# Optimization experiments

Measured on AMD Instinct MI355X. Metric: run time of the kernel, lower is better.

The kernel has to match this reference:

```python
import jax, jax.numpy as jnp
import numpy as np

D_MODEL = 1024
N_HEADS = 16
D_K = D_MODEL // N_HEADS
THETA = 10000.0
BATCH, SEQ = 2, 2048


def setup_inputs() -> dict:
    key = jax.random.key(0)
    k1, k2, k3 = jax.random.split(key, 3)
    std_qkv = float(np.sqrt(2.0 / (3 * D_MODEL + D_MODEL)))
    std_o = float(np.sqrt(2.0 / (D_MODEL + D_MODEL)))
    return {
        "x": jax.random.normal(k1, (BATCH, SEQ, D_MODEL), dtype=jnp.float32),
        "w_qkv": jax.random.normal(k2, (3 * D_MODEL, D_MODEL), dtype=jnp.float32) * std_qkv,
        "w_o": jax.random.normal(k3, (D_MODEL, D_MODEL), dtype=jnp.float32) * std_o,
        "token_positions": jnp.arange(SEQ, dtype=jnp.int32),
    }


def _rope(x, token_positions):
    # x: [..., s, d_k]; interleaved rotary embedding
    d_k = x.shape[-1]
    freqs = jnp.arange(0, d_k, 2, dtype=jnp.float32) / d_k          # [d_k/2]
    inv_freqs = 1.0 / (THETA ** freqs)
    angles = token_positions.astype(jnp.float32)[:, None] * inv_freqs  # [s, d_k/2]
    cos, sin = jnp.cos(angles), jnp.sin(angles)
    x_even, x_odd = x[..., 0::2], x[..., 1::2]
    rot_even = x_even * cos - x_odd * sin
    rot_odd = x_even * sin + x_odd * cos
    # interleave back: out[..., 2i] = rot_even[i], out[..., 2i+1] = rot_odd[i]
    return jnp.stack([rot_even, rot_odd], axis=-1).reshape(x.shape)


def reference(x, w_qkv, w_o, token_positions):
    b, s, _ = x.shape
    qkv = jnp.einsum('oi,bsi->bso', w_qkv, x)                        # [b, s, 3*d_model]
    q, k, v = jnp.split(qkv, 3, axis=-1)
    def to_heads(t):
        return t.reshape(b, s, N_HEADS, D_K).transpose(0, 2, 1, 3)  # [b, h, s, d]
    q, k, v = to_heads(q), to_heads(k), to_heads(v)
    q = _rope(q, token_positions)
    k = _rope(k, token_positions)
    scores = jnp.einsum('bhqd,bhkd->bhqk', q, k) / jnp.sqrt(jnp.float32(D_K))
    causal = jnp.tril(jnp.ones((s, s), dtype=bool))
    scores = jnp.where(causal, scores, -jnp.inf)
    attn = jax.nn.softmax(scores, axis=-1)
    y = jnp.einsum('bhqk,bhkd->bhqd', attn, v)
    y = y.transpose(0, 2, 1, 3).reshape(b, s, D_MODEL)
    return jnp.einsum('oi,bsi->bso', w_o, y)
```

## Files before the change

### kernel.cpp

```cpp
#include <hip/hip_runtime.h>
#include <math.h>

#define DEV __device__ __forceinline__

typedef __attribute__((ext_vector_type(8))) short bf16x8;
typedef __attribute__((ext_vector_type(4))) float f32x4;
typedef __attribute__((ext_vector_type(4))) unsigned int u32x4;

typedef __attribute__((address_space(3))) unsigned int lds_u32;
typedef const __attribute__((address_space(1))) unsigned int glb_u32;

DEV void gload16(const unsigned short* g, unsigned short* l) {
  __builtin_amdgcn_global_load_lds((glb_u32*)g, (lds_u32*)l, 16, 0, 0);
}

DEV bf16x8 lds_read8(const unsigned short* base, unsigned int byteoff) {
  return *reinterpret_cast<const bf16x8*>(
      reinterpret_cast<const char*>(base) + byteoff);
}

DEV float fexp2(float x) { return __builtin_amdgcn_exp2f(x); }

DEV unsigned short f2bf(float f) {
  union { float f; unsigned int u; } v; v.f = f;
  unsigned int u = v.u;
  unsigned int r = (u + 0x7fffu + ((u >> 16) & 1u)) >> 16;
  return (unsigned short)r;
}
DEV float bf2f(unsigned short h) {
  union { unsigned int u; float f; } v; v.u = ((unsigned int)h) << 16;
  return v.f;
}
DEV unsigned int cvtpk_bf16(float lo, float hi) {
  unsigned int r;
  asm("v_cvt_pk_bf16_f32 %0, %1, %2" : "=v"(r) : "v"(lo), "v"(hi));
  return r;
}

__global__ void cvt3_f32_bf16(const float* __restrict__ ina,
                              unsigned short* __restrict__ outa, int n4a,
                              const float* __restrict__ inb,
                              unsigned short* __restrict__ outb, int n4b,
                              const float* __restrict__ inc,
                              unsigned short* __restrict__ outc, int n4c) {
  int stride = gridDim.x * blockDim.x;
  int total = n4a + n4b + n4c;
  for (int i = blockIdx.x * blockDim.x + threadIdx.x; i < total; i += stride) {
    const float* src;
    unsigned short* dst;
    int j = i;
    if (j < n4a) {
      src = ina; dst = outa;
    } else if ((j -= n4a) < n4b) {
      src = inb; dst = outb;
    } else {
      j -= n4b; src = inc; dst = outc;
    }
    float4 f = reinterpret_cast<const float4*>(src)[j];
    ushort4 o;
    o.x = f2bf(f.x); o.y = f2bf(f.y); o.z = f2bf(f.z); o.w = f2bf(f.w);
    reinterpret_cast<ushort4*>(dst)[j] = o;
  }
}

__global__ __launch_bounds__(512, 2) void gemm8_qkv(const unsigned short* __restrict__ A,
                                                    const unsigned short* __restrict__ B,
                                                    unsigned short* __restrict__ C) {
  constexpr int K = 1024;
  constexpr int NK = 16;
  __shared__ unsigned short Ls[2][32768];

  const int tid = threadIdx.x;
  const int lane = tid & 63, wid = tid >> 6;
  const int wm = (wid >> 2) * 128;
  const int wn = (wid & 3) * 64;
  const int fr = lane & 15, kq = lane >> 4;

  int bid = blockIdx.x;
  int swz = (bid & 7) * 24 + (bid >> 3);
  int tm = swz & 15, tn = swz >> 4;
  const int arow0 = tm * 256, brow0 = tn * 256;

  const int subrow = lane >> 3;
  const int scol = ((lane & 7) ^ subrow) * 8;
  const unsigned short* aSrc = A + (size_t)(arow0 + wid * 8 + subrow) * K + scol;
  const unsigned short* bSrc = B + (size_t)(brow0 + wid * 8 + subrow) * K + scol;

  unsigned aoff[2], boff[2];
#pragma unroll
  for (int ks = 0; ks < 2; ks++) {
    unsigned x = ((unsigned)((ks * 4 + kq) ^ (fr & 7))) * 16;
    aoff[ks] = (unsigned)((wm + fr) * 128) + x;
    boff[ks] = 32768u + (unsigned)((wn + fr) * 128) + x;
  }

  f32x4 acc[8][4] = {};

#define STAGE_A8(BUF, H, T)                                                  \
  {                                                                          \
    gload16(aSrc + (size_t)((H) * 128) * K + (T) * 64,                       \
            &Ls[BUF][((H) * 128 + wid * 8) * 64]);                           \
    gload16(aSrc + (size_t)((H) * 128 + 64) * K + (T) * 64,                  \
            &Ls[BUF][((H) * 128 + 64 + wid * 8) * 64]);                      \
  }
#define STAGE_B8(BUF, H, T)                                                  \
  {                                                                          \
    gload16(bSrc + (size_t)((H) * 128) * K + (T) * 64,                       \
            &Ls[BUF][16384 + ((H) * 128 + wid * 8) * 64]);                   \
    gload16(bSrc + (size_t)((H) * 128 + 64) * K + (T) * 64,                  \
            &Ls[BUF][16384 + ((H) * 128 + 64 + wid * 8) * 64]);              \
  }

  STAGE_A8(0, 0, 0) STAGE_A8(0, 1, 0)
  STAGE_B8(0, 0, 0) STAGE_B8(0, 1, 0)
  STAGE_B8(1, 0, 1) STAGE_B8(1, 1, 1)
  asm volatile("s_waitcnt vmcnt(4)" ::: "memory");
  __builtin_amdgcn_s_barrier();

#define PHASE8(BUF, P, DO_STAGE)                                              \
  {                                                                           \
    bf16x8 af[2][2];                                                          \
    _Pragma("unroll") for (int mm = 0; mm < 2; mm++)                          \
      _Pragma("unroll") for (int ks = 0; ks < 2; ks++)                        \
        af[mm][ks] = lds_read8(Ls[BUF], aoff[ks] + ((P) * 2 + mm) * 2048);    \
    DO_STAGE                                                                  \
    __builtin_amdgcn_s_setprio(1);                                            \
    _Pragma("unroll") for (int mm = 0; mm < 2; mm++)                          \
      _Pragma("unroll") for (int j = 0; j < 4; j++)                           \
        _Pragma("unroll") for (int ks = 0; ks < 2; ks++)                      \
          acc[(P) * 2 + mm][j] = __builtin_amdgcn_mfma_f32_16x16x32_bf16(     \
              af[mm][ks], bq[j][ks], acc[(P) * 2 + mm][j], 0, 0, 0);          \
    __builtin_amdgcn_s_setprio(0);                                            \
  }

#define TILE8(T, BUF)                                                          \
  {                                                                            \
    bf16x8 bq[4][2];                                                           \
    _Pragma("unroll") for (int j = 0; j < 4; j++)                              \
      _Pragma("unroll") for (int ks = 0; ks < 2; ks++)                         \
        bq[j][ks] = lds_read8(Ls[BUF], boff[ks] + j * 2048);                   \
    PHASE8(BUF, 0, {                                                           \
      if ((T) + 1 < NK) { STAGE_A8(BUF ^ 1, 0, (T) + 1) STAGE_A8(BUF ^ 1, 1, (T) + 1) } \
    })                                                                         \
    __builtin_amdgcn_s_barrier();                                              \
    PHASE8(BUF, 1, { if ((T) + 2 < NK) STAGE_B8(BUF, 0, (T) + 2) })            \
    __builtin_amdgcn_s_barrier();                                              \
    PHASE8(BUF, 2, { if ((T) + 2 < NK) STAGE_B8(BUF, 1, (T) + 2) })            \
    __builtin_amdgcn_s_barrier();                                              \
    PHASE8(BUF, 3, {})                                                         \
    if ((T) + 2 < NK) {                                                        \
      asm volatile("s_waitcnt vmcnt(4)" ::: "memory");                         \
    } else {                                                                   \
      asm volatile("s_waitcnt vmcnt(0)" ::: "memory");                         \
    }                                                                          \
    __builtin_amdgcn_s_barrier();                                              \
    __builtin_amdgcn_sched_barrier(0);                                         \
  }

#pragma unroll 1
  for (int t = 0; t < NK; t += 2) {
    TILE8(t, 0)
    TILE8(t + 1, 1)
  }
#undef TILE8
#undef PHASE8
#undef STAGE_A8
#undef STAGE_B8

#pragma unroll
  for (int m = 0; m < 8; m++) {
#pragma unroll
    for (int j = 0; j < 4; j++) {
      size_t row = (size_t)(arow0 + wm + m * 16 + kq * 4);
      size_t col = (size_t)(brow0 + wn + j * 16 + fr);
#pragma unroll
      for (int r = 0; r < 4; r++)
        C[(row + r) * 3072 + col] = f2bf(acc[m][j][r]);
    }
  }
}

#define GEMM_PROLOGUE(A_, B_, K_)                                              \
  __shared__ unsigned short Ab[2][4096];                                       \
  __shared__ unsigned short Bb[2][4096];                                       \
  const int tid = threadIdx.x;                                                 \
  const int lane = tid & 63, wid = tid >> 6;                                   \
  const int wm = (wid >> 1) * 64, wn = (wid & 1) * 64;                         \
  const int fr = lane & 15, kq = lane >> 4;                                    \
  const int arow0 = blockIdx.x * 128;                                          \
  const int brow0 = blockIdx.y * 128;                                          \
  const int srow = wid * 16 + (lane >> 2);                                     \
  const int sslot = (((lane & 3) ^ ((lane >> 2) & 3))) * 8;                    \
  const unsigned short* aptr = (A_) + (size_t)(arow0 + srow) * (K_) + sslot;   \
  const unsigned short* bptr = (B_) + (size_t)(brow0 + srow) * (K_) + sslot;   \
  unsigned int offa[4], offb[4];                                               \
  _Pragma("unroll") for (int i = 0; i < 4; i++) {                              \
    offa[i] = (unsigned)((wm + i * 16 + fr) * 64 + ((kq ^ (fr & 3)) * 16));    \
    offb[i] = (unsigned)((wn + i * 16 + fr) * 64 + ((kq ^ (fr & 3)) * 16));    \
  }                                                                            \
  f32x4 acc[4][4] = {};

#define GSTAGE(BI, K_)                                             \
  {                                                                \
    gload16(aptr, &Ab[BI][wid * 512]);                             \
    gload16(aptr + (size_t)64 * (K_), &Ab[BI][2048 + wid * 512]);  \
    gload16(bptr, &Bb[BI][wid * 512]);                             \
    gload16(bptr + (size_t)64 * (K_), &Bb[BI][2048 + wid * 512]);  \
    aptr += 32;                                                    \
    bptr += 32;                                                    \
  }

#define GCOMP(BI)                                                                      \
  {                                                                                    \
    bf16x8 af[4], bfr[4];                                                              \
    _Pragma("unroll") for (int i = 0; i < 4; i++) af[i] = lds_read8(Ab[BI], offa[i]);  \
    _Pragma("unroll") for (int j = 0; j < 4; j++) bfr[j] = lds_read8(Bb[BI], offb[j]); \
    _Pragma("unroll") for (int i = 0; i < 4; i++)                                      \
      _Pragma("unroll") for (int j = 0; j < 4; j++)                                    \
        acc[i][j] = __builtin_amdgcn_mfma_f32_16x16x32_bf16(af[i], bfr[j], acc[i][j], 0, 0, 0); \
  }

#define GEMM_MAIN(K_)                       \
  {                                         \
    const int nk = (K_) >> 5;     \
    GSTAGE(0, K_);                          \
    for (int ks = 0; ks < nk; ks += 2) {    \
      __syncthreads();                      \
      GSTAGE(1, K_);                        \
      GCOMP(0);                             \
      __syncthreads();                      \
      if (ks + 2 < nk) GSTAGE(0, K_);       \
      GCOMP(1);                             \
    }                                       \
  }

template <bool BF16_OUT>
__global__ __launch_bounds__(256) void gemm_bt(const unsigned short* __restrict__ A,
                                               const unsigned short* __restrict__ B,
                                               void* __restrict__ Cv,
                                               int M, int N, int K) {
  GEMM_PROLOGUE(A, B, K)
  GEMM_MAIN(K)
#pragma unroll
  for (int i = 0; i < 4; i++) {
#pragma unroll
    for (int j = 0; j < 4; j++) {
#pragma unroll
      for (int r = 0; r < 4; r++) {
        size_t row = (size_t)(arow0 + wm + i * 16 + kq * 4 + r);
        size_t col = (size_t)(brow0 + wn + j * 16 + fr);
        if (BF16_OUT)
          ((unsigned short*)Cv)[row * N + col] = f2bf(acc[i][j][r]);
        else
          ((float*)Cv)[row * N + col] = acc[i][j][r];
      }
    }
  }
}

__global__ __launch_bounds__(256) void rope_kernel(unsigned short* __restrict__ qkv,
                                                   const int* __restrict__ pos) {
  int m = blockIdx.x;
  int s = m & 2047;
  int t = threadIdx.x;
  __shared__ float Cl[32], Sl[32];
  if (t < 32) {
    float position = (float)pos[s];
    float inv = __expf(-(float)t * (9.210340371976184f / 32.0f));
    float ang = position * inv;
    Cl[t] = cosf(ang);
    Sl[t] = sinf(ang);
  }
  __syncthreads();
  const float QS = 0.18033688011112042f;
  int h = t >> 4, g = t & 15;
  float c0 = Cl[2 * g], s0 = Sl[2 * g], c1 = Cl[2 * g + 1], s1 = Sl[2 * g + 1];
  size_t base = (size_t)m * 3072 + h * 64 + 4 * g;
  ushort4 qv = *reinterpret_cast<ushort4*>(&qkv[base]);
  float qe0 = bf2f(qv.x), qo0 = bf2f(qv.y), qe1 = bf2f(qv.z), qo1 = bf2f(qv.w);
  qv.x = f2bf((qe0 * c0 - qo0 * s0) * QS);
  qv.y = f2bf((qe0 * s0 + qo0 * c0) * QS);
  qv.z = f2bf((qe1 * c1 - qo1 * s1) * QS);
  qv.w = f2bf((qe1 * s1 + qo1 * c1) * QS);
  *reinterpret_cast<ushort4*>(&qkv[base]) = qv;
  size_t kb = base + 1024;
  ushort4 kv = *reinterpret_cast<ushort4*>(&qkv[kb]);
  float ke0 = bf2f(kv.x), ko0 = bf2f(kv.y), ke1 = bf2f(kv.z), ko1 = bf2f(kv.w);
  kv.x = f2bf(ke0 * c0 - ko0 * s0);
  kv.y = f2bf(ke0 * s0 + ko0 * c0);
  kv.z = f2bf(ke1 * c1 - ko1 * s1);
  kv.w = f2bf(ke1 * s1 + ko1 * c1);
  *reinterpret_cast<ushort4*>(&qkv[kb]) = kv;
}

__global__ __launch_bounds__(256) void vtrans_kernel(const unsigned short* __restrict__ qkv,
                                                     unsigned short* __restrict__ vt) {
  int bid = blockIdx.x;
  int sb = bid & 31;
  int bh = bid >> 5;
  int h = bh & 15, b = bh >> 4;
  __shared__ unsigned short tile[64][72];
  int t = threadIdx.x;
  int sl = t >> 2, c0 = (t & 3) * 16;
  const unsigned short* src = qkv + (size_t)(b * 2048 + sb * 64) * 3072 + 2048 + h * 64;
  *reinterpret_cast<bf16x8*>(&tile[sl][c0]) =
      *reinterpret_cast<const bf16x8*>(&src[(size_t)sl * 3072 + c0]);
  *reinterpret_cast<bf16x8*>(&tile[sl][c0 + 8]) =
      *reinterpret_cast<const bf16x8*>(&src[(size_t)sl * 3072 + c0 + 8]);
  __syncthreads();
  int d = t >> 2, p0 = (t & 3) * 16;
  unsigned short* dst = vt + ((size_t)bh * 64 + d) * 2048 + sb * 64 + p0;
  bf16x8 o0, o1;
#pragma unroll
  for (int i = 0; i < 8; i++) {
    int p = p0 + i;
    int s_in = (p & 32) + ((p >> 2) & 1) * 16 + ((p >> 3) & 3) * 4 + (p & 3);
    o0[i] = (short)tile[s_in][d];
  }
#pragma unroll
  for (int i = 0; i < 8; i++) {
    int p = p0 + 8 + i;
    int s_in = (p & 32) + ((p >> 2) & 1) * 16 + ((p >> 3) & 3) * 4 + (p & 3);
    o1[i] = (short)tile[s_in][d];
  }
  *reinterpret_cast<bf16x8*>(dst) = o0;
  *reinterpret_cast<bf16x8*>(dst + 8) = o1;
}

__global__ __launch_bounds__(512, 2) void attn_kernel(const unsigned short* __restrict__ qkv,
                                                      const unsigned short* __restrict__ vt,
                                                      unsigned short* __restrict__ Y) {
  int bid = blockIdx.x;
  int bh = bid & 31;
  int j = bid >> 5;
  int qt = (j < 8) ? (15 - j) : (j - 8);
  int h = bh & 15, b = bh >> 4;
  int tid = threadIdx.x, lane = tid & 63, wid = tid >> 6;
  int fr = lane & 15, kq = lane >> 4;
  int qbase = qt * 128 + wid * 16;

  const size_t mrow0 = (size_t)b * 2048;
  const unsigned short* Qp = qkv + (mrow0 + qbase) * 3072 + h * 64;
  const unsigned short* Kp = qkv + mrow0 * 3072 + 1024 + h * 64;
  const unsigned short* Vp = vt + ((size_t)bh * 64) * 2048;

  __shared__ unsigned short Klds[2][4096];
  __shared__ unsigned short Vlds[2][4096];

  bf16x8 qf[2];
#pragma unroll
  for (int ks = 0; ks < 2; ks++)
    qf[ks] = *reinterpret_cast<const bf16x8*>(&Qp[(size_t)fr * 3072 + ks * 32 + kq * 8]);

  const int srow = tid >> 3;
  const int schunk = (tid & 7) ^ (srow & 7);
  const unsigned short* kstage = Kp + (size_t)srow * 3072 + schunk * 8;
  const unsigned short* vstage = Vp + (size_t)srow * 2048 + schunk * 8;

  unsigned int offk[8], offv[8];
#pragma unroll
  for (int g = 0; g < 4; g++)
#pragma unroll
    for (int ks = 0; ks < 2; ks++) {
      int R = g * 16 + fr;
      offk[g * 2 + ks] = (unsigned)(R * 128 + (((4 * ks + kq) ^ (R & 7)) * 16));
    }
#pragma unroll
  for (int db = 0; db < 4; db++)
#pragma unroll
    for (int hf = 0; hf < 2; hf++) {
      int d = db * 16 + fr;
      offv[db * 2 + hf] = (unsigned)(d * 128 + (((4 * hf + kq) ^ (d & 7)) * 16));
    }

  bf16x8 vones;
#pragma unroll
  for (int i = 0; i < 8; i++) vones[i] = (short)0x3F80;

  f32x4 acc[4] = {};
  f32x4 lacc = {};
  const int q_lane = qbase + fr;
  const int ntiles = 2 * qt + 2;
  const int mask_from = qbase >> 6;
  const int t_skip = (qbase + 79) >> 6;

#define STAGE(BI)                                 \
  {                                               \
    gload16(kstage, &Klds[BI][wid * 512]);        \
    gload16(vstage, &Vlds[BI][wid * 512]);        \
    kstage += (size_t)64 * 3072;                  \
    vstage += 64;                                 \
  }

#define TILE_COMPUTE(T, BI)                                                           \
  if ((T) < t_skip) {                                                                 \
    const bool masked_ = ((T) >= mask_from);                                          \
    f32x4 sc[4] = {};                                                                 \
    __builtin_amdgcn_s_setprio(1);                                                    \
    _Pragma("unroll") for (int g = 0; g < 4; g++) {                                   \
      _Pragma("unroll") for (int ks = 0; ks < 2; ks++) {                              \
        bf16x8 kf = lds_read8(Klds[BI], offk[g * 2 + ks]);                            \
        sc[g] = __builtin_amdgcn_mfma_f32_16x16x32_bf16(kf, qf[ks], sc[g], 0, 0, 0);  \
      }                                                                               \
    }                                                                                 \
    __builtin_amdgcn_s_setprio(0);                                                    \
    float p[16];                                                                      \
    _Pragma("unroll") for (int g = 0; g < 4; g++)                                     \
      _Pragma("unroll") for (int r = 0; r < 4; r++) {                                 \
        float v = sc[g][r];                                                           \
        if (masked_) {                                                                \
          int k = (T) * 64 + g * 16 + kq * 4 + r;                                     \
          if (k > q_lane) v = -1e30f;                                                 \
        }                                                                             \
        p[g * 4 + r] = fexp2(v);                                                      \
      }                                                                               \
    u32x4 W0 = {cvtpk_bf16(p[0], p[1]), cvtpk_bf16(p[2], p[3]),                       \
                cvtpk_bf16(p[4], p[5]), cvtpk_bf16(p[6], p[7])};                      \
    u32x4 W1 = {cvtpk_bf16(p[8], p[9]), cvtpk_bf16(p[10], p[11]),                     \
                cvtpk_bf16(p[12], p[13]), cvtpk_bf16(p[14], p[15])};                  \
    bf16x8 pa0 = *reinterpret_cast<bf16x8*>(&W0);                                     \
    bf16x8 pa1 = *reinterpret_cast<bf16x8*>(&W1);                                     \
    __builtin_amdgcn_s_setprio(1);                                                    \
    _Pragma("unroll") for (int db = 0; db < 4; db++) {                                \
      bf16x8 vf0 = lds_read8(Vlds[BI], offv[db * 2]);                                 \
      acc[db] = __builtin_amdgcn_mfma_f32_16x16x32_bf16(vf0, pa0, acc[db], 0, 0, 0);  \
      bf16x8 vf1 = lds_read8(Vlds[BI], offv[db * 2 + 1]);                             \
      acc[db] = __builtin_amdgcn_mfma_f32_16x16x32_bf16(vf1, pa1, acc[db], 0, 0, 0);  \
    }                                                                                 \
    lacc = __builtin_amdgcn_mfma_f32_16x16x32_bf16(vones, pa0, lacc, 0, 0, 0);        \
    lacc = __builtin_amdgcn_mfma_f32_16x16x32_bf16(vones, pa1, lacc, 0, 0, 0);        \
    __builtin_amdgcn_s_setprio(0);                                                    \
  }

  STAGE(0);
  for (int t = 0; t < ntiles; t += 2) {
    __syncthreads();
    if (t + 1 < ntiles) STAGE(1);
    TILE_COMPUTE(t, 0);
    if (t + 1 >= ntiles) break;
    __syncthreads();
    if (t + 2 < ntiles) STAGE(0);
    TILE_COMPUTE(t + 1, 1);
  }
#undef TILE_COMPUTE
#undef STAGE

  float inv = 1.0f / lacc[0];
  unsigned short* yp = Y + (mrow0 + qbase + fr) * 1024 + h * 64 + kq * 4;
#pragma unroll
  for (int db = 0; db < 4; db++) {
    ushort4 o;
    o.x = f2bf(acc[db][0] * inv);
    o.y = f2bf(acc[db][1] * inv);
    o.z = f2bf(acc[db][2] * inv);
    o.w = f2bf(acc[db][3] * inv);
    *reinterpret_cast<ushort4*>(yp + db * 16) = o;
  }
}

extern "C" void kernel_launch(void* const* d_in, const int* in_sizes, int n_in,
                              void* d_out, int out_size, void* d_ws, size_t ws_size,
                              hipStream_t stream) {
  const float* x     = (const float*)d_in[0];
  const float* w_qkv = (const float*)d_in[1];
  const float* w_o   = (const float*)d_in[2];
  const int*   pos   = (const int*)d_in[3];
  float* out = (float*)d_out;

  unsigned char* ws = (unsigned char*)d_ws;
  unsigned short* x_bf    = (unsigned short*)(ws);
  unsigned short* wqkv_bf = (unsigned short*)(ws + 8388608);
  unsigned short* wo_bf   = (unsigned short*)(ws + 14680064);
  unsigned short* qkv     = (unsigned short*)(ws + 16777216);
  unsigned short* vt      = (unsigned short*)(ws + 41943040);
  unsigned short* y       = (unsigned short*)(ws + 50331648);

  cvt3_f32_bf16<<<1536, 256, 0, stream>>>(x, x_bf, 4096 * 1024 / 4,
                                          w_qkv, wqkv_bf, 3072 * 1024 / 4,
                                          w_o, wo_bf, 1024 * 1024 / 4);

  gemm8_qkv<<<192, 512, 0, stream>>>(x_bf, wqkv_bf, qkv);

  rope_kernel<<<4096, 256, 0, stream>>>(qkv, pos);
  vtrans_kernel<<<1024, 256, 0, stream>>>(qkv, vt);

  attn_kernel<<<512, 512, 0, stream>>>(qkv, vt, y);

  gemm_bt<false><<<dim3(32, 8), 256, 0, stream>>>(y, wo_bf, (void*)out, 4096, 1024, 1024);
}
```

Baseline: 121.7 us.

## Merge rope and V-transpose kernels, retile attention, use explicit waitcnt pipelining

Rope and V-transpose now run as one launch, which saves a kernel launch. Attention moves from 512-thread blocks over 128-query tiles to 256-thread blocks over 64-query tiles, with 1024 blocks scheduled in descending query-tile order. That removes the old skip/mask bookkeeping and staging is adjusted to match. Both the output GEMM and attention replace __syncthreads with manual s_waitcnt vmcnt/lgkmcnt plus s_barrier, so the next stage's global loads stay in flight while the current tile computes. The manual waitcnt counts are fragile and risk races if the load counts change.

```diff
diff --git a/kernel.cpp b/kernel.cpp
--- a/kernel.cpp
+++ b/kernel.cpp
@@ -180,32 +180,37 @@
   }
 }
 
-#define GEMM_PROLOGUE(A_, B_, K_)                                              \
-  __shared__ unsigned short Ab[2][4096];                                       \
-  __shared__ unsigned short Bb[2][4096];                                       \
-  const int tid = threadIdx.x;                                                 \
-  const int lane = tid & 63, wid = tid >> 6;                                   \
-  const int wm = (wid >> 1) * 64, wn = (wid & 1) * 64;                         \
-  const int fr = lane & 15, kq = lane >> 4;                                    \
-  const int arow0 = blockIdx.x * 128;                                          \
-  const int brow0 = blockIdx.y * 128;                                          \
-  const int srow = wid * 16 + (lane >> 2);                                     \
-  const int sslot = (((lane & 3) ^ ((lane >> 2) & 3))) * 8;                    \
-  const unsigned short* aptr = (A_) + (size_t)(arow0 + srow) * (K_) + sslot;   \
-  const unsigned short* bptr = (B_) + (size_t)(brow0 + srow) * (K_) + sslot;   \
-  unsigned int offa[4], offb[4];                                               \
-  _Pragma("unroll") for (int i = 0; i < 4; i++) {                              \
-    offa[i] = (unsigned)((wm + i * 16 + fr) * 64 + ((kq ^ (fr & 3)) * 16));    \
-    offb[i] = (unsigned)((wn + i * 16 + fr) * 64 + ((kq ^ (fr & 3)) * 16));    \
-  }                                                                            \
+template <bool BF16_OUT>
+__global__ __launch_bounds__(256) void gemm_bt(const unsigned short* __restrict__ A,
+                                               const unsigned short* __restrict__ B,
+                                               void* __restrict__ Cv,
+                                               int M, int N, int K) {
+  __shared__ unsigned short Ab[2][4096];
+  __shared__ unsigned short Bb[2][4096];
+  const int tid = threadIdx.x;
+  const int lane = tid & 63, wid = tid >> 6;
+  const int wm = (wid >> 1) * 64, wn = (wid & 1) * 64;
+  const int fr = lane & 15, kq = lane >> 4;
+  const int arow0 = blockIdx.x * 128;
+  const int brow0 = blockIdx.y * 128;
+  const int srow = wid * 16 + (lane >> 2);
+  const int sslot = (((lane & 3) ^ ((lane >> 2) & 3))) * 8;
+  const unsigned short* aptr = A + (size_t)(arow0 + srow) * K + sslot;
+  const unsigned short* bptr = B + (size_t)(brow0 + srow) * K + sslot;
+  unsigned int offa[4], offb[4];
+#pragma unroll
+  for (int i = 0; i < 4; i++) {
+    offa[i] = (unsigned)((wm + i * 16 + fr) * 64 + ((kq ^ (fr & 3)) * 16));
+    offb[i] = (unsigned)((wn + i * 16 + fr) * 64 + ((kq ^ (fr & 3)) * 16));
+  }
   f32x4 acc[4][4] = {};
 
-#define GSTAGE(BI, K_)                                             \
+#define GSTAGE(BI)                                                 \
   {                                                                \
     gload16(aptr, &Ab[BI][wid * 512]);                             \
-    gload16(aptr + (size_t)64 * (K_), &Ab[BI][2048 + wid * 512]);  \
+    gload16(aptr + (size_t)64 * K, &Ab[BI][2048 + wid * 512]);     \
     gload16(bptr, &Bb[BI][wid * 512]);                             \
-    gload16(bptr + (size_t)64 * (K_), &Bb[BI][2048 + wid * 512]);  \
+    gload16(bptr + (size_t)64 * K, &Bb[BI][2048 + wid * 512]);     \
     aptr += 32;                                                    \
     bptr += 32;                                                    \
   }
@@ -220,27 +225,27 @@
         acc[i][j] = __builtin_amdgcn_mfma_f32_16x16x32_bf16(af[i], bfr[j], acc[i][j], 0, 0, 0); \
   }
 
-#define GEMM_MAIN(K_)                       \
-  {                                         \
-    const int nk = (K_) >> 5;     \
-    GSTAGE(0, K_);                          \
-    for (int ks = 0; ks < nk; ks += 2) {    \
-      __syncthreads();                      \
-      GSTAGE(1, K_);                        \
-      GCOMP(0);                             \
-      __syncthreads();                      \
-      if (ks + 2 < nk) GSTAGE(0, K_);       \
-      GCOMP(1);                             \
-    }                                       \
-  }
-
-template <bool BF16_OUT>
-__global__ __launch_bounds__(256) void gemm_bt(const unsigned short* __restrict__ A,
-                                               const unsigned short* __restrict__ B,
-                                               void* __restrict__ Cv,
-                                               int M, int N, int K) {
-  GEMM_PROLOGUE(A, B, K)
-  GEMM_MAIN(K)
+  const int nk = K >> 5;
+  GSTAGE(0);
+  for (int ks = 0; ks < nk; ks += 2) {
+    asm volatile("s_waitcnt lgkmcnt(0)" ::: "memory");
+    __builtin_amdgcn_s_barrier();
+    GSTAGE(1);
+    asm volatile("s_waitcnt vmcnt(4)" ::: "memory");
+    GCOMP(0);
+    asm volatile("s_waitcnt lgkmcnt(0)" ::: "memory");
+    __builtin_amdgcn_s_barrier();
+    if (ks + 2 < nk) {
+      GSTAGE(0);
+      asm volatile("s_waitcnt vmcnt(4)" ::: "memory");
+    } else {
+      asm volatile("s_waitcnt vmcnt(0)" ::: "memory");
+    }
+    GCOMP(1);
+  }
+#undef GSTAGE
+#undef GCOMP
+
 #pragma unroll
   for (int i = 0; i < 4; i++) {
 #pragma unroll
@@ -258,86 +263,85 @@
   }
 }
 
-__global__ __launch_bounds__(256) void rope_kernel(unsigned short* __restrict__ qkv,
-                                                   const int* __restrict__ pos) {
-  int m = blockIdx.x;
-  int s = m & 2047;
+__global__ __launch_bounds__(256) void rope_vtrans_kernel(unsigned short* __restrict__ qkv,
+                                                          const int* __restrict__ pos,
+                                                          unsigned short* __restrict__ vt) {
+  int bid0 = blockIdx.x;
   int t = threadIdx.x;
-  __shared__ float Cl[32], Sl[32];
-  if (t < 32) {
-    float position = (float)pos[s];
-    float inv = __expf(-(float)t * (9.210340371976184f / 32.0f));
-    float ang = position * inv;
-    Cl[t] = cosf(ang);
-    Sl[t] = sinf(ang);
-  }
-  __syncthreads();
-  const float QS = 0.18033688011112042f;
-  int h = t >> 4, g = t & 15;
-  float c0 = Cl[2 * g], s0 = Sl[2 * g], c1 = Cl[2 * g + 1], s1 = Sl[2 * g + 1];
-  size_t base = (size_t)m * 3072 + h * 64 + 4 * g;
-  ushort4 qv = *reinterpret_cast<ushort4*>(&qkv[base]);
-  float qe0 = bf2f(qv.x), qo0 = bf2f(qv.y), qe1 = bf2f(qv.z), qo1 = bf2f(qv.w);
-  qv.x = f2bf((qe0 * c0 - qo0 * s0) * QS);
-  qv.y = f2bf((qe0 * s0 + qo0 * c0) * QS);
-  qv.z = f2bf((qe1 * c1 - qo1 * s1) * QS);
-  qv.w = f2bf((qe1 * s1 + qo1 * c1) * QS);
-  *reinterpret_cast<ushort4*>(&qkv[base]) = qv;
-  size_t kb = base + 1024;
-  ushort4 kv = *reinterpret_cast<ushort4*>(&qkv[kb]);
-  float ke0 = bf2f(kv.x), ko0 = bf2f(kv.y), ke1 = bf2f(kv.z), ko1 = bf2f(kv.w);
-  kv.x = f2bf(ke0 * c0 - ko0 * s0);
-  kv.y = f2bf(ke0 * s0 + ko0 * c0);
-  kv.z = f2bf(ke1 * c1 - ko1 * s1);
-  kv.w = f2bf(ke1 * s1 + ko1 * c1);
-  *reinterpret_cast<ushort4*>(&qkv[kb]) = kv;
-}
-
-__global__ __launch_bounds__(256) void vtrans_kernel(const unsigned short* __restrict__ qkv,
-                                                     unsigned short* __restrict__ vt) {
-  int bid = blockIdx.x;
-  int sb = bid & 31;
-  int bh = bid >> 5;
-  int h = bh & 15, b = bh >> 4;
-  __shared__ unsigned short tile[64][72];
-  int t = threadIdx.x;
-  int sl = t >> 2, c0 = (t & 3) * 16;
-  const unsigned short* src = qkv + (size_t)(b * 2048 + sb * 64) * 3072 + 2048 + h * 64;
-  *reinterpret_cast<bf16x8*>(&tile[sl][c0]) =
-      *reinterpret_cast<const bf16x8*>(&src[(size_t)sl * 3072 + c0]);
-  *reinterpret_cast<bf16x8*>(&tile[sl][c0 + 8]) =
-      *reinterpret_cast<const bf16x8*>(&src[(size_t)sl * 3072 + c0 + 8]);
-  __syncthreads();
-  int d = t >> 2, p0 = (t & 3) * 16;
-  unsigned short* dst = vt + ((size_t)bh * 64 + d) * 2048 + sb * 64 + p0;
-  bf16x8 o0, o1;
-#pragma unroll
-  for (int i = 0; i < 8; i++) {
-    int p = p0 + i;
-    int s_in = (p & 32) + ((p >> 2) & 1) * 16 + ((p >> 3) & 3) * 4 + (p & 3);
-    o0[i] = (short)tile[s_in][d];
-  }
-#pragma unroll
-  for (int i = 0; i < 8; i++) {
-    int p = p0 + 8 + i;
-    int s_in = (p & 32) + ((p >> 2) & 1) * 16 + ((p >> 3) & 3) * 4 + (p & 3);
-    o1[i] = (short)tile[s_in][d];
-  }
-  *reinterpret_cast<bf16x8*>(dst) = o0;
-  *reinterpret_cast<bf16x8*>(dst + 8) = o1;
-}
-
-__global__ __launch_bounds__(512, 2) void attn_kernel(const unsigned short* __restrict__ qkv,
+  if (bid0 < 4096) {
+    int m = bid0;
+    int s = m & 2047;
+    __shared__ float Cl[32], Sl[32];
+    if (t < 32) {
+      float position = (float)pos[s];
+      float inv = __expf(-(float)t * (9.210340371976184f / 32.0f));
+      float ang = position * inv;
+      Cl[t] = cosf(ang);
+      Sl[t] = sinf(ang);
+    }
+    __syncthreads();
+    const float QS = 0.18033688011112042f;
+    int h = t >> 4, g = t & 15;
+    float c0 = Cl[2 * g], s0 = Sl[2 * g], c1 = Cl[2 * g + 1], s1 = Sl[2 * g + 1];
+    size_t base = (size_t)m * 3072 + h * 64 + 4 * g;
+    ushort4 qv = *reinterpret_cast<ushort4*>(&qkv[base]);
+    float qe0 = bf2f(qv.x), qo0 = bf2f(qv.y), qe1 = bf2f(qv.z), qo1 = bf2f(qv.w);
+    qv.x = f2bf((qe0 * c0 - qo0 * s0) * QS);
+    qv.y = f2bf((qe0 * s0 + qo0 * c0) * QS);
+    qv.z = f2bf((qe1 * c1 - qo1 * s1) * QS);
+    qv.w = f2bf((qe1 * s1 + qo1 * c1) * QS);
+    *reinterpret_cast<ushort4*>(&qkv[base]) = qv;
+    size_t kb = base + 1024;
+    ushort4 kv = *reinterpret_cast<ushort4*>(&qkv[kb]);
+    float ke0 = bf2f(kv.x), ko0 = bf2f(kv.y), ke1 = bf2f(kv.z), ko1 = bf2f(kv.w);
+    kv.x = f2bf(ke0 * c0 - ko0 * s0);
+    kv.y = f2bf(ke0 * s0 + ko0 * c0);
+    kv.z = f2bf(ke1 * c1 - ko1 * s1);
+    kv.w = f2bf(ke1 * s1 + ko1 * c1);
+    *reinterpret_cast<ushort4*>(&qkv[kb]) = kv;
+  } else {
+    int bid = bid0 - 4096;
+    int sb = bid & 31;
+    int bh = bid >> 5;
+    int h = bh & 15, b = bh >> 4;
+    __shared__ unsigned short tile[64][72];
+    int sl = t >> 2, c0 = (t & 3) * 16;
+    const unsigned short* src = qkv + (size_t)(b * 2048 + sb * 64) * 3072 + 2048 + h * 64;
+    *reinterpret_cast<bf16x8*>(&tile[sl][c0]) =
+        *reinterpret_cast<const bf16x8*>(&src[(size_t)sl * 3072 + c0]);
+    *reinterpret_cast<bf16x8*>(&tile[sl][c0 + 8]) =
+        *reinterpret_cast<const bf16x8*>(&src[(size_t)sl * 3072 + c0 + 8]);
+    __syncthreads();
+    int d = t >> 2, p0 = (t & 3) * 16;
+    unsigned short* dst = vt + ((size_t)bh * 64 + d) * 2048 + sb * 64 + p0;
+    bf16x8 o0, o1;
+#pragma unroll
+    for (int i = 0; i < 8; i++) {
+      int p = p0 + i;
+      int s_in = (p & 32) + ((p >> 2) & 1) * 16 + ((p >> 3) & 3) * 4 + (p & 3);
+      o0[i] = (short)tile[s_in][d];
+    }
+#pragma unroll
+    for (int i = 0; i < 8; i++) {
+      int p = p0 + 8 + i;
+      int s_in = (p & 32) + ((p >> 2) & 1) * 16 + ((p >> 3) & 3) * 4 + (p & 3);
+      o1[i] = (short)tile[s_in][d];
+    }
+    *reinterpret_cast<bf16x8*>(dst) = o0;
+    *reinterpret_cast<bf16x8*>(dst + 8) = o1;
+  }
+}
+
+__global__ __launch_bounds__(256, 4) void attn_kernel(const unsigned short* __restrict__ qkv,
                                                       const unsigned short* __restrict__ vt,
                                                       unsigned short* __restrict__ Y) {
   int bid = blockIdx.x;
   int bh = bid & 31;
-  int j = bid >> 5;
-  int qt = (j < 8) ? (15 - j) : (j - 8);
+  int qt = 31 - (bid >> 5);
   int h = bh & 15, b = bh >> 4;
   int tid = threadIdx.x, lane = tid & 63, wid = tid >> 6;
   int fr = lane & 15, kq = lane >> 4;
-  int qbase = qt * 128 + wid * 16;
+  int qbase = qt * 64 + wid * 16;
 
   const size_t mrow0 = (size_t)b * 2048;
   const unsigned short* Qp = qkv + (mrow0 + qbase) * 3072 + h * 64;
@@ -380,21 +384,21 @@
   f32x4 acc[4] = {};
   f32x4 lacc = {};
   const int q_lane = qbase + fr;
-  const int ntiles = 2 * qt + 2;
-  const int mask_from = qbase >> 6;
-  const int t_skip = (qbase + 79) >> 6;
-
-#define STAGE(BI)                                 \
-  {                                               \
-    gload16(kstage, &Klds[BI][wid * 512]);        \
-    gload16(vstage, &Vlds[BI][wid * 512]);        \
-    kstage += (size_t)64 * 3072;                  \
-    vstage += 64;                                 \
+  const int ntiles = qt + 1;
+
+#define STAGE(BI)                                                     \
+  {                                                                   \
+    gload16(kstage, &Klds[BI][wid * 512]);                            \
+    gload16(kstage + (size_t)32 * 3072, &Klds[BI][2048 + wid * 512]); \
+    gload16(vstage, &Vlds[BI][wid * 512]);                            \
+    gload16(vstage + 32 * 2048, &Vlds[BI][2048 + wid * 512]);         \
+    kstage += (size_t)64 * 3072;                                      \
+    vstage += 64;                                                     \
   }
 
 #define TILE_COMPUTE(T, BI)                                                           \
-  if ((T) < t_skip) {                                                                 \
-    const bool masked_ = ((T) >= mask_from);                                          \
+  {                                                                                   \
+    const bool masked_ = ((T) == qt);                                                 \
     f32x4 sc[4] = {};                                                                 \
     __builtin_amdgcn_s_setprio(1);                                                    \
     _Pragma("unroll") for (int g = 0; g < 4; g++) {                                   \
@@ -434,12 +438,24 @@
 
   STAGE(0);
   for (int t = 0; t < ntiles; t += 2) {
-    __syncthreads();
-    if (t + 1 < ntiles) STAGE(1);
+    asm volatile("s_waitcnt lgkmcnt(0)" ::: "memory");
+    __builtin_amdgcn_s_barrier();
+    if (t + 1 < ntiles) {
+      STAGE(1);
+      asm volatile("s_waitcnt vmcnt(4)" ::: "memory");
+    } else {
+      asm volatile("s_waitcnt vmcnt(0)" ::: "memory");
+    }
     TILE_COMPUTE(t, 0);
     if (t + 1 >= ntiles) break;
-    __syncthreads();
-    if (t + 2 < ntiles) STAGE(0);
+    asm volatile("s_waitcnt lgkmcnt(0)" ::: "memory");
+    __builtin_amdgcn_s_barrier();
+    if (t + 2 < ntiles) {
+      STAGE(0);
+      asm volatile("s_waitcnt vmcnt(4)" ::: "memory");
+    } else {
+      asm volatile("s_waitcnt vmcnt(0)" ::: "memory");
+    }
     TILE_COMPUTE(t + 1, 1);
   }
 #undef TILE_COMPUTE
@@ -481,10 +497,9 @@
 
   gemm8_qkv<<<192, 512, 0, stream>>>(x_bf, wqkv_bf, qkv);
 
-  rope_kernel<<<4096, 256, 0, stream>>>(qkv, pos);
-  vtrans_kernel<<<1024, 256, 0, stream>>>(qkv, vt);
-
-  attn_kernel<<<512, 512, 0, stream>>>(qkv, vt, y);
+  rope_vtrans_kernel<<<5120, 256, 0, stream>>>(qkv, pos, vt);
+
+  attn_kernel<<<1024, 256, 0, stream>>>(qkv, vt, y);
 
   gemm_bt<false><<<dim3(32, 8), 256, 0, stream>>>(y, wo_bf, (void*)out, 4096, 1024, 1024);
 }
```

Result: faster. 114.0 us (-6.4%).
